# Optimization experiments

Measured on AMD Instinct MI355X. Metric: run time of the kernel, lower is better.

## Reference

```python
import jax, jax.numpy as jnp
import numpy as np
import math

H, C = 16, 4


def _clustering(x, alv, mu, log_var, log_prior, mi_estimation):
    # x: [B,h,L,D], alv: [B,h,L], mu/log_var: [h or 1, C, D], log_prior: [h or 1, C]
    B, Hh, L, D = x.shape
    z = x  # eval mode: no reparameterization noise
    zd = z[:, :, :, None, :]                       # [B,h,L,1,D]
    mu_b = mu[:, None, :, :]                       # [h,1,C,D]
    lv = log_var[:, None, :, :]
    var = jnp.exp(lv)
    lp = jax.nn.log_softmax(log_prior, axis=-1)    # [h,C]
    mse = (zd - mu_b) ** 2 / var                   # [B,h,L,C,D]
    log_pdf = -0.5 * mse.sum(-1) - 0.5 * lv.sum(-1) - D * math.pi  # [B,h,L,C]
    log_pdf = log_pdf + lp[:, None, :]
    shift = jax.lax.stop_gradient(log_pdf.max(axis=-1, keepdims=True))
    log_probs = jax.nn.log_softmax(log_pdf - shift + 5.0, axis=-1)
    cp = jnp.exp(log_probs)                        # cluster probs [B,h,L,C]
    lp_b = jnp.broadcast_to(lp[None, :, None, :], log_probs.shape)
    # F.kl_div(log_probs, prior) = prior * (log prior - log_probs)
    kl = (jnp.exp(lp_b) * (lp_b - log_probs)).sum(-1).mean(axis=(1, 2))
    alv5 = alv[:, :, :, None, None]
    avar = jnp.exp(alv5)
    kl = kl + 0.5 * (cp * (mse + avar / var + lv).sum(-1)).sum(-1).mean(axis=(1, 2))
    kl = kl - 0.5 * ((1.0 + alv5).sum(-1) * D).mean(axis=(1, 2, 3))
    eye = jnp.eye(L, dtype=x.dtype)
    div = jnp.einsum('bhqc,bhkc->bhqk', cp, cp)
    div = ((div - eye) ** 2) * (eye * 1.25 + (1.0 - eye) * 0.75)
    div_loss = div.mean(axis=(1, 2, 3))
    if mi_estimation:
        pdf = jnp.exp(log_pdf - jax.lax.stop_gradient(log_pdf.max())).sum(-1, keepdims=True)
        w = cp * pdf
        mi_probs = w / jnp.maximum(w.sum(axis=2, keepdims=True), 1e-6)  # L1 normalize over L
        mi_p = jnp.minimum(jnp.einsum('bilc,bjlc->blij', mi_probs, cp), 1.0)
        mask_h = 1.0 - jnp.eye(Hh, dtype=x.dtype)
        mi_loss = -(jnp.log(1.0 - mi_p + 1e-6) * mask_h).mean(axis=(1, 2, 3)) * 10.0
        aff = jnp.einsum('bhqc,bhkc->bhqk', cp, cp)
        diag = jnp.diagonal(jax.nn.log_softmax(aff, axis=-1), axis1=2, axis2=3)
        mi_loss = mi_loss - diag.mean(axis=(1, 2))
    else:
        mi_loss = jnp.zeros_like(kl)
    return z, cp, kl, div_loss, mi_loss


def _forward(query, key, value, Wq, bq, Wk, bk, Wv, bv, Wo, bo, Wsem, bsem,
             Whead, bhead, tok_mu, tok_log_var, tok_log_prior,
             head_mu, head_log_var, head_log_prior):
    B, L, D = query.shape
    Dk = D // H
    q = query @ Wq + bq
    k = key @ Wk + bk
    v = value @ Wv + bv
    alv = (q @ Wsem + bsem).transpose(0, 2, 1)                 # [B,H,L]
    qh = q.reshape(B, L, H, Dk).transpose(0, 2, 1, 3)          # [B,H,L,Dk]
    z, cp_q, kl_q, div_q, _ = _clustering(qh, alv, tok_mu, tok_log_var, tok_log_prior, False)
    kh = k.reshape(B, L, H, Dk).transpose(0, 2, 1, 3)
    vh = v.reshape(B, L, H, Dk).transpose(0, 2, 1, 3)
    cluster_mask = jnp.einsum('bhqc,bhkc->bhqk', cp_q, cp_q)   # token-cluster affinity mask
    scores = jnp.einsum('bhqd,bhkd->bhqk', z, kh) / math.sqrt(Dk)
    attn = jax.nn.softmax(scores, axis=-1) * cluster_mask
    attn = attn / (attn.sum(axis=-1, keepdims=True) + 1e-6)
    ctx = jnp.einsum('bhqk,bhkd->bhqd', attn, vh)              # [B,H,L,Dk]
    ctx_f = ctx.transpose(0, 2, 1, 3).reshape(B, L, D)
    alv_h = (ctx_f @ Whead + bhead).transpose(0, 2, 1)         # [B,H,L]
    _, cp_h, kl_h, div_h, mi = _clustering(ctx, alv_h, head_mu, head_log_var, head_log_prior, True)
    out = ctx_f @ Wo + bo
    return out, attn.mean(axis=1), kl_q + kl_h, div_q + div_h, mi


def setup_inputs() -> dict:
    key = jax.random.key(0)
    ks = jax.random.split(key, 12)
    B, L, D = 8, 512, 1024
    Dk = D // H
    s = 1.0 / math.sqrt(D)
    f32 = jnp.float32
    inp = {
        'query': jax.random.normal(ks[0], (B, L, D), f32),
        'key': jax.random.normal(ks[1], (B, L, D), f32),
        'value': jax.random.normal(ks[2], (B, L, D), f32),
        'Wq': jax.random.normal(ks[3], (D, D), f32) * s, 'bq': jnp.zeros((D,), f32),
        'Wk': jax.random.normal(ks[4], (D, D), f32) * s, 'bk': jnp.zeros((D,), f32),
        'Wv': jax.random.normal(ks[5], (D, D), f32) * s, 'bv': jnp.zeros((D,), f32),
        'Wo': jax.random.normal(ks[6], (D, D), f32) * s, 'bo': jnp.zeros((D,), f32),
        'Wsem': jax.random.normal(ks[7], (D, H), f32) * s, 'bsem': jnp.zeros((H,), f32),
        'Whead': jax.random.normal(ks[8], (D, H), f32) * s, 'bhead': jnp.zeros((H,), f32),
        'tok_mu': jax.random.normal(ks[9], (H, C, Dk), f32) * 0.1,
        'tok_log_var': jnp.zeros((H, C, Dk), f32),
        'tok_log_prior': jnp.full((H, C), math.log(1.0 / C), f32),
        'head_mu': jax.random.normal(ks[10], (1, C, Dk), f32) * 0.1,
        'head_log_var': jnp.zeros((1, C, Dk), f32),
        'head_log_prior': jnp.full((1, C), math.log(1.0 / C), f32),
    }
    return inp


def reference(query, key, value, Wq, bq, Wk, bk, Wv, bv, Wo, bo, Wsem, bsem,
              Whead, bhead, tok_mu, tok_log_var, tok_log_prior,
              head_mu, head_log_var, head_log_prior):
    return _forward(query, key, value, Wq, bq, Wk, bk, Wv, bv, Wo, bo, Wsem, bsem,
                    Whead, bhead, tok_mu, tok_log_var, tok_log_prior,
                    head_mu, head_log_var, head_log_prior)
```

## Files before the change

### kernel.cpp

```cpp
#include <hip/hip_runtime.h>
#include <math.h>

#define BB 8
#define LL 512
#define DD 1024
#define HH 16
#define CC 4
#define DK 64
#define NEG_DPI 201.06192982974676f

typedef __attribute__((ext_vector_type(8))) short short8;
typedef __attribute__((ext_vector_type(4))) float floatx4;
typedef __attribute__((ext_vector_type(8))) unsigned short u16x8;
typedef __attribute__((ext_vector_type(4))) unsigned short u16x4;

__device__ inline float block_sum256(float v, float* s_red) {
    int t = threadIdx.x;
    s_red[t] = v; __syncthreads();
    for (int off = 128; off > 0; off >>= 1) {
        if (t < off) s_red[t] += s_red[t + off];
        __syncthreads();
    }
    float r = s_red[0]; __syncthreads();
    return r;
}
__device__ inline float block_max256(float v, float* s_red) {
    int t = threadIdx.x;
    s_red[t] = v; __syncthreads();
    for (int off = 128; off > 0; off >>= 1) {
        if (t < off) s_red[t] = fmaxf(s_red[t], s_red[t + off]);
        __syncthreads();
    }
    float r = s_red[0]; __syncthreads();
    return r;
}
__device__ inline unsigned int fenc(float f) {
    unsigned int b = __float_as_uint(f);
    return (b & 0x80000000u) ? ~b : (b | 0x80000000u);
}
__device__ inline float fdec(unsigned int u) {
    return (u & 0x80000000u) ? __uint_as_float(u ^ 0x80000000u) : __uint_as_float(~u);
}
__device__ inline unsigned short f2bf(float x) {
    unsigned int u = __float_as_uint(x);
    return (unsigned short)((u + 0x7FFFu + ((u >> 16) & 1u)) >> 16);
}
__device__ inline float bf2f(unsigned short h) {
    return __uint_as_float((unsigned int)h << 16);
}

__global__ __launch_bounds__(256)
void convert_hilo(const float* __restrict__ x, unsigned short* __restrict__ hh,
                  unsigned short* __restrict__ ll) {
    int i = blockIdx.x * 256 + threadIdx.x;
    float4 v = ((const float4*)x)[i];
    u16x4 h, l;
    float c[4] = {v.x, v.y, v.z, v.w};
#pragma unroll
    for (int j = 0; j < 4; j++) {
        unsigned short hb = f2bf(c[j]);
        h[j] = hb;
        l[j] = f2bf(c[j] - bf2f(hb));
    }
    ((u16x4*)hh)[i] = h;
    ((u16x4*)ll)[i] = l;
}

__global__ __launch_bounds__(256)
void wconv4(const float* __restrict__ W0, const float* __restrict__ W1,
            const float* __restrict__ W2, const float* __restrict__ W3,
            unsigned short* __restrict__ Tbase) {
    __shared__ float tile[64][65];
    int z = blockIdx.z;
    const float* W = (z == 0) ? W0 : (z == 1) ? W1 : (z == 2) ? W2 : W3;
    const size_t WS = (size_t)DD * DD;
    unsigned short* Th = Tbase + (size_t)z * 2 * WS;
    unsigned short* Tl = Th + WS;
    int t = threadIdx.x;
    int n0 = blockIdx.x * 64, k0 = blockIdx.y * 64;
    int r = t >> 4, c4 = (t & 15) * 4;
#pragma unroll
    for (int rr = 0; rr < 64; rr += 16) {
        float4 v = *(const float4*)&W[(size_t)(k0 + r + rr) * DD + n0 + c4];
        tile[r + rr][c4 + 0] = v.x; tile[r + rr][c4 + 1] = v.y;
        tile[r + rr][c4 + 2] = v.z; tile[r + rr][c4 + 3] = v.w;
    }
    __syncthreads();
    int rn = t >> 2, kg = (t & 3) * 16;
    u16x8 oh[2], ol[2];
#pragma unroll
    for (int j = 0; j < 16; j++) {
        float x = tile[kg + j][rn];
        unsigned short hb = f2bf(x);
        oh[j >> 3][j & 7] = hb;
        ol[j >> 3][j & 7] = f2bf(x - bf2f(hb));
    }
    size_t o = (size_t)(n0 + rn) * DD + k0 + kg;
    *(u16x8*)&Th[o] = oh[0]; *(u16x8*)&Th[o + 8] = oh[1];
    *(u16x8*)&Tl[o] = ol[0]; *(u16x8*)&Tl[o + 8] = ol[1];
}

__device__ __forceinline__
void gemm_body(const unsigned short* __restrict__ Ah, const unsigned short* __restrict__ Al,
               const unsigned short* __restrict__ Bh, const unsigned short* __restrict__ Bl,
               const float* __restrict__ bias, float* __restrict__ C,
               unsigned short* __restrict__ Ch, unsigned short* __restrict__ Cl,
               int m0, int n0) {
    __shared__ unsigned short sAh[128 * 32];
    __shared__ unsigned short sAl[128 * 32];
    __shared__ unsigned short sBh[128 * 32];
    __shared__ unsigned short sBl[128 * 32];
    int t = threadIdx.x;
    int lane = t & 63, w = t >> 6;
    int wm = w >> 1, wn = w & 1;
    int lm = lane & 15, quad = lane >> 4;
    int srow = t >> 1, sk = (t & 1) * 16;

    const unsigned short* gAh = Ah + (size_t)(m0 + srow) * DD + sk;
    const unsigned short* gAl = Al + (size_t)(m0 + srow) * DD + sk;
    const unsigned short* gBh = Bh + (size_t)(n0 + srow) * DD + sk;
    const unsigned short* gBl = Bl + (size_t)(n0 + srow) * DD + sk;
    int f = (srow >> 1) & 3;
    int s0 = (t & 1) * 2;
    int ws0 = srow * 32 + ((s0 ^ f) * 8);
    int ws1 = srow * 32 + (((s0 | 1) ^ f) * 8);

    floatx4 acc[4][4] = {};
    u16x8 a0, a1, a2, a3, b0, b1, b2, b3;
    a0 = *(const u16x8*)(gAh);     a1 = *(const u16x8*)(gAh + 8);
    a2 = *(const u16x8*)(gAl);     a3 = *(const u16x8*)(gAl + 8);
    b0 = *(const u16x8*)(gBh);     b1 = *(const u16x8*)(gBh + 8);
    b2 = *(const u16x8*)(gBl);     b3 = *(const u16x8*)(gBl + 8);

    for (int kt = 0; kt < 32; kt++) {
        __syncthreads();
        *(u16x8*)&sAh[ws0] = a0; *(u16x8*)&sAh[ws1] = a1;
        *(u16x8*)&sAl[ws0] = a2; *(u16x8*)&sAl[ws1] = a3;
        *(u16x8*)&sBh[ws0] = b0; *(u16x8*)&sBh[ws1] = b1;
        *(u16x8*)&sBl[ws0] = b2; *(u16x8*)&sBl[ws1] = b3;
        __syncthreads();
        if (kt < 31) {
            int kb = (kt + 1) * 32;
            a0 = *(const u16x8*)(gAh + kb); a1 = *(const u16x8*)(gAh + kb + 8);
            a2 = *(const u16x8*)(gAl + kb); a3 = *(const u16x8*)(gAl + kb + 8);
            b0 = *(const u16x8*)(gBh + kb); b1 = *(const u16x8*)(gBh + kb + 8);
            b2 = *(const u16x8*)(gBl + kb); b3 = *(const u16x8*)(gBl + kb + 8);
        }

        short8 bhf[4], blf[4];
#pragma unroll
        for (int j = 0; j < 4; j++) {
            int nrow = wn * 64 + j * 16 + lm;
            int nb = nrow * 32 + ((quad ^ ((nrow >> 1) & 3)) * 8);
            bhf[j] = *(const short8*)&sBh[nb];
            blf[j] = *(const short8*)&sBl[nb];
        }
#pragma unroll
        for (int i = 0; i < 4; i++) {
            int arow = wm * 64 + i * 16 + lm;
            int ab = arow * 32 + ((quad ^ ((arow >> 1) & 3)) * 8);
            short8 ah = *(const short8*)&sAh[ab];
            short8 al = *(const short8*)&sAl[ab];
#pragma unroll
            for (int j = 0; j < 4; j++) {
                acc[i][j] = __builtin_amdgcn_mfma_f32_16x16x32_bf16(ah, bhf[j], acc[i][j], 0, 0, 0);
                acc[i][j] = __builtin_amdgcn_mfma_f32_16x16x32_bf16(ah, blf[j], acc[i][j], 0, 0, 0);
                acc[i][j] = __builtin_amdgcn_mfma_f32_16x16x32_bf16(al, bhf[j], acc[i][j], 0, 0, 0);
            }
        }
    }
#pragma unroll
    for (int i = 0; i < 4; i++) {
#pragma unroll
        for (int j = 0; j < 4; j++) {
            int n = n0 + wn * 64 + j * 16 + lm;
            float bv = bias[n];
#pragma unroll
            for (int r = 0; r < 4; r++) {
                int m = m0 + wm * 64 + i * 16 + quad * 4 + r;
                size_t idx = (size_t)m * DD + n;
                float val = acc[i][j][r] + bv;
                if (C) C[idx] = val;
                if (Ch) {
                    unsigned short hb = f2bf(val);
                    Ch[idx] = hb;
                    Cl[idx] = f2bf(val - bf2f(hb));
                }
            }
        }
    }
}

__global__ __launch_bounds__(256)
void mfma_gemm_bias(const unsigned short* __restrict__ Ah, const unsigned short* __restrict__ Al,
                    const unsigned short* __restrict__ Bh, const unsigned short* __restrict__ Bl,
                    const float* __restrict__ bias, float* __restrict__ C,
                    unsigned short* __restrict__ Ch, unsigned short* __restrict__ Cl) {
    int id = blockIdx.x;
    int xcd = id & 7, s = id >> 3;
    int y = xcd * 4 + (s >> 3);
    int x = s & 7;
    gemm_body(Ah, Al, Bh, Bl, bias, C, Ch, Cl, y * 128, x * 128);
}

__global__ __launch_bounds__(256)
void mfma_gemm_qkv(const unsigned short* __restrict__ ist3, const unsigned short* __restrict__ wbase,
                   const float* __restrict__ bq, const float* __restrict__ bk,
                   const float* __restrict__ bv, float* __restrict__ Cq,
                   unsigned short* __restrict__ obase) {
    int id = blockIdx.x;
    int xcd = id & 7, s = id >> 3;
    int p = xcd * 12 + (s >> 3);
    int x = s & 7;
    int z = p >> 5;
    int y = p & 31;
    const size_t NB = (size_t)BB * LL * DD;
    const size_t WS = (size_t)DD * DD;
    const unsigned short* Ah = ist3 + (size_t)z * 2 * NB;
    const unsigned short* Bh = wbase + (size_t)z * 2 * WS;
    const float* bias = (z == 0) ? bq : (z == 1) ? bk : bv;
    float* C = (z == 0) ? Cq : nullptr;
    unsigned short* Ch = obase + (size_t)z * 2 * NB;
    gemm_body(Ah, Ah + NB, Bh, Bh + WS, bias, C, Ch, Ch + NB, y * 128, x * 128);
}

__global__ __launch_bounds__(256)
void vt_prep2(const unsigned short* __restrict__ voh, const unsigned short* __restrict__ vol,
              unsigned short* __restrict__ vth, unsigned short* __restrict__ vtl) {
    __shared__ unsigned short tile[128 * 68];
    int t = threadIdx.x;
    int which = blockIdx.x & 1;
    int l0 = (blockIdx.x >> 1) * 128, h = blockIdx.y, b = blockIdx.z;
    const unsigned short* src = which ? vol : voh;
    unsigned short* dst = which ? vtl : vth;
#pragma unroll
    for (int i = 0; i < 8; i++) {
        int u = t + i * 256;
        int l = u >> 4, c4 = (u & 15) * 4;
        u16x4 v4 = *(const u16x4*)&src[((size_t)(b * LL + l0 + l)) * DD + h * DK + c4];
        tile[l * 68 + c4 + 0] = v4[0]; tile[l * 68 + c4 + 1] = v4[1];
        tile[l * 68 + c4 + 2] = v4[2]; tile[l * 68 + c4 + 3] = v4[3];
    }
    __syncthreads();
    size_t ob = ((size_t)(b * HH + h)) * DK * LL;
#pragma unroll
    for (int i = 0; i < 8; i++) {
        int u = t + i * 256;
        int d = u >> 5, lq = (u & 31) * 4;
        u16x4 o;
#pragma unroll
        for (int j = 0; j < 4; j++) o[j] = tile[(lq + j) * 68 + d];
        *(u16x4*)&dst[ob + (size_t)d * LL + l0 + lq] = o;
    }
}

__global__ __launch_bounds__(256)
void alv_gemm(const float* __restrict__ A, const float* __restrict__ Wp,
              const float* __restrict__ bias, float* __restrict__ alv) {
    __shared__ float As[16][65];
    __shared__ float Ws[64][17];
    int t = threadIdx.x;
    int m0 = blockIdx.x * 16;
    int r = t >> 4, hh = t & 15;
    float acc = 0.f;
    for (int kt = 0; kt < 16; kt++) {
        __syncthreads();
#pragma unroll
        for (int i = 0; i < 4; i++) {
            int e = t + i * 256;
            int rr = e >> 6, kk = e & 63;
            As[rr][kk] = A[(size_t)(m0 + rr) * DD + kt * 64 + kk];
        }
#pragma unroll
        for (int i = 0; i < 4; i++) {
            int e = t + i * 256;
            int kk = e >> 4, h2 = e & 15;
            Ws[kk][h2] = Wp[(size_t)(kt * 64 + kk) * HH + h2];
        }
        __syncthreads();
#pragma unroll
        for (int kk = 0; kk < 64; kk++) acc += As[r][kk] * Ws[kk][hh];
    }
    int m = m0 + r;
    int b = m >> 9, l = m & 511;
    alv[(size_t)(b * HH + hh) * LL + l] = acc + bias[hh];
}

__global__ __launch_bounds__(256)
void cluster_kernel(const float* __restrict__ zsrc, const float* __restrict__ alv,
                    const float* __restrict__ mu, const float* __restrict__ logvar,
                    const float* __restrict__ logprior,
                    float* __restrict__ cp_out, float* __restrict__ lpdf_out,
                    unsigned int* __restrict__ maxenc, float* __restrict__ kl_out,
                    int isHead) {
    __shared__ float s_mu[CC * DK], s_iv[CC * DK], s_lv[CC * DK];
    __shared__ float s_slv[CC], s_siv[CC], s_lp[CC];
    __shared__ float s_red[256];
    int t = threadIdx.x;
    int tile = blockIdx.x & 1;
    int bh = blockIdx.x >> 1;
    int h = bh & (HH - 1), b = bh >> 4;
    int hm = isHead ? 0 : h;

    {
        float m = mu[hm * CC * DK + t];
        float lv = logvar[hm * CC * DK + t];
        s_mu[t] = m; s_lv[t] = lv; s_iv[t] = expf(-lv);
    }
    __syncthreads();
    if (t < CC) {
        float slv = 0.f, siv = 0.f;
        for (int d = 0; d < DK; d++) { slv += s_lv[t * DK + d]; siv += s_iv[t * DK + d]; }
        s_slv[t] = slv; s_siv[t] = siv;
    }
    if (t == CC) {
        float x[CC];
        float m = -1e30f;
        for (int c = 0; c < CC; c++) { x[c] = logprior[hm * CC + c]; m = fmaxf(m, x[c]); }
        float se = 0.f;
        for (int c = 0; c < CC; c++) se += expf(x[c] - m);
        float lse = m + logf(se);
        for (int c = 0; c < CC; c++) s_lp[c] = x[c] - lse;
    }
    __syncthreads();

    int l = tile * 256 + t;
    const float* zp = zsrc + ((size_t)(b * LL + l)) * DD + h * DK;
    float acc[CC] = {0.f, 0.f, 0.f, 0.f};
    for (int d = 0; d < DK; d += 4) {
        float4 z4 = *(const float4*)(zp + d);
#pragma unroll
        for (int c = 0; c < CC; c++) {
            float d0 = z4.x - s_mu[c * DK + d];     acc[c] += d0 * d0 * s_iv[c * DK + d];
            float d1 = z4.y - s_mu[c * DK + d + 1]; acc[c] += d1 * d1 * s_iv[c * DK + d + 1];
            float d2 = z4.z - s_mu[c * DK + d + 2]; acc[c] += d2 * d2 * s_iv[c * DK + d + 2];
            float d3 = z4.w - s_mu[c * DK + d + 3]; acc[c] += d3 * d3 * s_iv[c * DK + d + 3];
        }
    }
    float lpdf[CC];
#pragma unroll
    for (int c = 0; c < CC; c++)
        lpdf[c] = -0.5f * acc[c] - 0.5f * s_slv[c] - NEG_DPI + s_lp[c];
    float m = fmaxf(fmaxf(lpdf[0], lpdf[1]), fmaxf(lpdf[2], lpdf[3]));
    float se = 0.f;
#pragma unroll
    for (int c = 0; c < CC; c++) se += expf(lpdf[c] - m);
    float lse = m + logf(se);
    float lprob[CC], cpv[CC];
    size_t idx = ((size_t)(bh * LL + l)) * CC;
#pragma unroll
    for (int c = 0; c < CC; c++) {
        lprob[c] = lpdf[c] - lse;
        cpv[c] = expf(lprob[c]);
        cp_out[idx + c] = cpv[c];
    }
    if (isHead) {
#pragma unroll
        for (int c = 0; c < CC; c++) lpdf_out[idx + c] = lpdf[c];
    }
    float alvv = alv[(size_t)bh * LL + l];
    float avar = expf(alvv);
    float t1 = 0.f, t2 = 0.f;
#pragma unroll
    for (int c = 0; c < CC; c++) {
        t1 += expf(s_lp[c]) * (s_lp[c] - lprob[c]);
        t2 += cpv[c] * (acc[c] + avar * s_siv[c] + s_slv[c]);
    }
    float klv = t1 + 0.5f * t2 - 0.5f * (float)DK * (1.0f + alvv);
    float tot = block_sum256(klv, s_red);
    if (t == 0) atomicAdd(kl_out + b, tot * (1.0f / (HH * LL)));
    if (isHead) {
        float mt = block_max256(m, s_red);
        if (t == 0) atomicMax(maxenc, fenc(mt));
    }
}

__global__ __launch_bounds__(256)
void pairstats_kernel(const float* __restrict__ cp, float* __restrict__ div_out,
                      float* __restrict__ mi_out, int isHead) {
    __shared__ float s_cp[LL * CC];
    __shared__ float s_red[256];
    int t = threadIdx.x;
    int bh = blockIdx.x >> 3;
    int seg = blockIdx.x & 7;
    int b = bh >> 4;
    const float* base = cp + (size_t)bh * LL * CC;
#pragma unroll
    for (int i = 0; i < 2; i++) {
        int e = t + i * 256;
        *(float4*)&s_cp[e * 4] = *(const float4*)&base[e * 4];
    }
    __syncthreads();

    int q = seg * 64 + (t >> 2);
    int ln = t & 3;
    float4 cq = *(float4*)&s_cp[q * 4];
    float divacc = 0.f, m = -1e30f, s = 0.f, selfdot = 0.f;
    for (int k = ln; k < LL; k += 4) {
        float4 ck = *(float4*)&s_cp[k * 4];
        float dot = cq.x * ck.x + cq.y * ck.y + cq.z * ck.z + cq.w * ck.w;
        float del = (k == q) ? 1.f : 0.f;
        float dd = dot - del;
        divacc += dd * dd * (0.75f + 0.5f * del);
        if (isHead) {
            if (dot > m) { s = s * expf(m - dot) + 1.f; m = dot; }
            else         { s += expf(dot - m); }
            if (k == q) selfdot = dot;
        }
    }
#pragma unroll
    for (int off = 1; off <= 2; off <<= 1) divacc += __shfl_xor(divacc, off, 64);
    float diag = 0.f;
    if (isHead) {
#pragma unroll
        for (int off = 1; off <= 2; off <<= 1) {
            float om = __shfl_xor(m, off, 64);
            float os = __shfl_xor(s, off, 64);
            float nm = fmaxf(m, om);
            s = s * expf(m - nm) + os * expf(om - nm);
            m = nm;
        }
#pragma unroll
        for (int off = 1; off <= 2; off <<= 1) selfdot += __shfl_xor(selfdot, off, 64);
        diag = selfdot - (m + logf(s));
    }
    float dtot = block_sum256(ln == 0 ? divacc : 0.f, s_red);
    if (t == 0) atomicAdd(div_out + b, dtot * (1.0f / ((float)HH * LL * LL)));
    if (isHead) {
        float gtot = block_sum256(ln == 0 ? diag : 0.f, s_red);
        if (t == 0) atomicAdd(mi_out + b, -gtot * (1.0f / (HH * LL)));
    }
}

__global__ __launch_bounds__(256)
void attn3_kernel(const unsigned short* __restrict__ qoh, const unsigned short* __restrict__ qol,
                  const unsigned short* __restrict__ koh, const unsigned short* __restrict__ kol,
                  const unsigned short* __restrict__ vth, const unsigned short* __restrict__ vtl,
                  const float* __restrict__ cpq,
                  float* __restrict__ ctxf, unsigned short* __restrict__ cxh,
                  unsigned short* __restrict__ cxl,
                  float* __restrict__ attn_h, int h0) {
    __shared__ __align__(16) char sbuf[33280];
    __shared__ float s_inv[16];
    float* S = (float*)sbuf;
    unsigned short* Ph = (unsigned short*)sbuf;
    unsigned short* Pl = Ph + 16 * 520;

    int t = threadIdx.x;
    int id = blockIdx.x;
    int xcd = id & 7;
    int sid = id >> 3;
    int qt = sid & 31;
    int combo = ((sid >> 5) << 3) | xcd;
    int hl = combo & 7;
    int b = combo >> 3;
    int h = h0 + hl;
    int q0 = qt * 16;
    int lane = t & 63, w = t >> 6;
    int lm = lane & 15, quad = lane >> 4;
    int bh = b * HH + h;

    size_t qbase = ((size_t)(b * LL + q0 + lm)) * DD + h * DK + quad * 8;
    short8 qah0 = *(const short8*)(qoh + qbase);
    short8 qah1 = *(const short8*)(qoh + qbase + 32);
    short8 qal0 = *(const short8*)(qol + qbase);
    short8 qal1 = *(const short8*)(qol + qbase + 32);

    floatx4 sa[8] = {};
#pragma unroll
    for (int j = 0; j < 8; j++) {
        int n0 = w * 128 + j * 16;
        size_t kbase = ((size_t)(b * LL + n0 + lm)) * DD + h * DK + quad * 8;
        short8 kbh0 = *(const short8*)(koh + kbase);
        short8 kbh1 = *(const short8*)(koh + kbase + 32);
        short8 kbl0 = *(const short8*)(kol + kbase);
        short8 kbl1 = *(const short8*)(kol + kbase + 32);
        sa[j] = __builtin_amdgcn_mfma_f32_16x16x32_bf16(qah0, kbh0, sa[j], 0, 0, 0);
        sa[j] = __builtin_amdgcn_mfma_f32_16x16x32_bf16(qah1, kbh1, sa[j], 0, 0, 0);
        sa[j] = __builtin_amdgcn_mfma_f32_16x16x32_bf16(qah0, kbl0, sa[j], 0, 0, 0);
        sa[j] = __builtin_amdgcn_mfma_f32_16x16x32_bf16(qah1, kbl1, sa[j], 0, 0, 0);
        sa[j] = __builtin_amdgcn_mfma_f32_16x16x32_bf16(qal0, kbh0, sa[j], 0, 0, 0);
        sa[j] = __builtin_amdgcn_mfma_f32_16x16x32_bf16(qal1, kbh1, sa[j], 0, 0, 0);
    }
#pragma unroll
    for (int j = 0; j < 8; j++) {
        int kc = w * 128 + j * 16 + lm;
#pragma unroll
        for (int r = 0; r < 4; r++)
            S[(quad * 4 + r) * 516 + kc] = sa[j][r] * 0.125f;
    }
    __syncthreads();

    {
        int r = t >> 4, ln = t & 15;
        const float4* cpb = (const float4*)(cpq + (size_t)bh * LL * CC);
        float m = -1e30f;
        for (int k = ln; k < LL; k += 16) m = fmaxf(m, S[r * 516 + k]);
#pragma unroll
        for (int off = 8; off > 0; off >>= 1) m = fmaxf(m, __shfl_xor(m, off, 16));
        float4 cq = cpb[q0 + r];
        float Z = 0.f, Sm = 0.f;
        for (int k = ln; k < LL; k += 16) {
            float e = expf(S[r * 516 + k] - m);
            float4 ck = cpb[k];
            float mask = cq.x * ck.x + cq.y * ck.y + cq.z * ck.z + cq.w * ck.w;
            float a = e * mask;
            Z += e; Sm += a;
            S[r * 516 + k] = a;
        }
#pragma unroll
        for (int off = 8; off > 0; off >>= 1) {
            Z += __shfl_xor(Z, off, 16);
            Sm += __shfl_xor(Sm, off, 16);
        }
        if (ln == 0) s_inv[r] = 1.f / (Sm + 1e-6f * Z);
    }
    __syncthreads();

    float4 pv[8];
#pragma unroll
    for (int i = 0; i < 8; i++) {
        int e = t + i * 256;
        int r2 = e >> 7, k4 = (e & 127) * 4;
        float4 p = *(float4*)&S[r2 * 516 + k4];
        float inv = s_inv[r2];
        p.x *= inv; p.y *= inv; p.z *= inv; p.w *= inv;
        pv[i] = p;
        *(float4*)&attn_h[(((size_t)((b * 8 + hl) * LL + q0 + r2)) * LL) + k4] = p;
    }
    __syncthreads();
#pragma unroll
    for (int i = 0; i < 8; i++) {
        int e = t + i * 256;
        int r2 = e >> 7, k4 = (e & 127) * 4;
        float c[4] = {pv[i].x, pv[i].y, pv[i].z, pv[i].w};
        u16x4 hv, lv;
#pragma unroll
        for (int j = 0; j < 4; j++) {
            unsigned short hb = f2bf(c[j]);
            hv[j] = hb;
            lv[j] = f2bf(c[j] - bf2f(hb));
        }
        *(u16x4*)&Ph[r2 * 520 + k4] = hv;
        *(u16x4*)&Pl[r2 * 520 + k4] = lv;
    }
    __syncthreads();

    int dn = w * 16 + lm;
    const unsigned short* vrh = vth + ((size_t)bh * DK + dn) * LL;
    const unsigned short* vrl = vtl + ((size_t)bh * DK + dn) * LL;
    floatx4 ca = {};
#pragma unroll
    for (int kc = 0; kc < 16; kc++) {
        int kb = kc * 32 + quad * 8;
        short8 pah = *(const short8*)&Ph[lm * 520 + kb];
        short8 pal = *(const short8*)&Pl[lm * 520 + kb];
        short8 vbh = *(const short8*)(vrh + kb);
        short8 vbl = *(const short8*)(vrl + kb);
        ca = __builtin_amdgcn_mfma_f32_16x16x32_bf16(pah, vbh, ca, 0, 0, 0);
        ca = __builtin_amdgcn_mfma_f32_16x16x32_bf16(pah, vbl, ca, 0, 0, 0);
        ca = __builtin_amdgcn_mfma_f32_16x16x32_bf16(pal, vbh, ca, 0, 0, 0);
    }
#pragma unroll
    for (int r = 0; r < 4; r++) {
        float val = ca[r];
        size_t idx = ((size_t)(b * LL + q0 + quad * 4 + r)) * DD + h * DK + dn;
        ctxf[idx] = val;
        unsigned short hb = f2bf(val);
        cxh[idx] = hb;
        cxl[idx] = f2bf(val - bf2f(hb));
    }
}

__global__ __launch_bounds__(256)
void attn_reduce(const float* __restrict__ attn_h, float* __restrict__ attn_out,
                 int accumulate) {
    int e = blockIdx.x * 256 + threadIdx.x;
    int b = e >> 16;
    int rem = e & 65535;
    float4 s = {0.f, 0.f, 0.f, 0.f};
#pragma unroll
    for (int hl = 0; hl < 8; hl++) {
        float4 v = ((const float4*)attn_h)[(((size_t)(b * 8 + hl)) << 16) + rem];
        s.x += v.x; s.y += v.y; s.z += v.z; s.w += v.w;
    }
    float4* o = (float4*)attn_out + (((size_t)b) << 16) + rem;
    const float sc = 1.0f / (float)HH;
    float4 prev = {0.f, 0.f, 0.f, 0.f};
    if (accumulate) prev = *o;
    prev.x += s.x * sc; prev.y += s.y * sc; prev.z += s.z * sc; prev.w += s.w * sc;
    *o = prev;
}

__global__ __launch_bounds__(256)
void wsum_kernel(const float* __restrict__ lpdf, const float* __restrict__ cp,
                 const unsigned int* __restrict__ maxenc,
                 float* __restrict__ pdf_out, float* __restrict__ wsum_out) {
    __shared__ float s_red[256];
    int t = threadIdx.x;
    int bh = blockIdx.x;
    float M = fdec(*maxenc);
    float a[CC] = {0.f, 0.f, 0.f, 0.f};
    for (int li = 0; li < 2; li++) {
        int l = t + li * 256;
        size_t idx = ((size_t)bh * LL + l) * CC;
        float p0 = expf(lpdf[idx + 0] - M);
        float p1 = expf(lpdf[idx + 1] - M);
        float p2 = expf(lpdf[idx + 2] - M);
        float p3 = expf(lpdf[idx + 3] - M);
        float pd = p0 + p1 + p2 + p3;
        pdf_out[(size_t)bh * LL + l] = pd;
        a[0] += cp[idx + 0] * pd; a[1] += cp[idx + 1] * pd;
        a[2] += cp[idx + 2] * pd; a[3] += cp[idx + 3] * pd;
    }
#pragma unroll
    for (int c = 0; c < CC; c++) {
        float tot = block_sum256(a[c], s_red);
        if (t == 0) wsum_out[bh * CC + c] = tot;
    }
}

__global__ __launch_bounds__(256)
void mi_kernel(const float* __restrict__ cp, const float* __restrict__ pdf,
               const float* __restrict__ wsum, float* __restrict__ mi_out) {
    __shared__ float s_q[HH * CC];
    __shared__ float s_c[HH * CC];
    __shared__ float s_red[256];
    int t = threadIdx.x;
    int b = blockIdx.x >> 9;
    int l = blockIdx.x & 511;
    if (t < HH * CC) {
        int i = t >> 2, c = t & 3;
        float cpv = cp[((size_t)(b * HH + i) * LL + l) * CC + c];
        s_c[t] = cpv;
        float w = cpv * pdf[(size_t)(b * HH + i) * LL + l];
        float ws = wsum[(b * HH + i) * CC + c];
        s_q[t] = w / fmaxf(ws, 1e-6f);
    }
    __syncthreads();
    int i = t >> 4, j = t & 15;
    float sdot = 0.f;
#pragma unroll
    for (int c = 0; c < CC; c++) sdot += s_q[i * 4 + c] * s_c[j * 4 + c];
    float mi_p = fminf(sdot, 1.f);
    float val = (i != j) ? logf(1.f - mi_p + 1e-6f) : 0.f;
    float tot = block_sum256(val, s_red);
    if (t == 0) atomicAdd(mi_out + b, -10.f * tot * (1.0f / ((float)LL * HH * HH)));
}

extern "C" void kernel_launch(void* const* d_in, const int* in_sizes, int n_in,
                              void* d_out, int out_size, void* d_ws, size_t ws_size,
                              hipStream_t stream) {
    (void)in_sizes; (void)n_in; (void)out_size; (void)ws_size;
    const float* query  = (const float*)d_in[0];
    const float* key    = (const float*)d_in[1];
    const float* value  = (const float*)d_in[2];
    const float* Wq     = (const float*)d_in[3];
    const float* bq     = (const float*)d_in[4];
    const float* Wk     = (const float*)d_in[5];
    const float* bk     = (const float*)d_in[6];
    const float* Wv     = (const float*)d_in[7];
    const float* bv     = (const float*)d_in[8];
    const float* Wo     = (const float*)d_in[9];
    const float* bo     = (const float*)d_in[10];
    const float* Wsem   = (const float*)d_in[11];
    const float* bsem   = (const float*)d_in[12];
    const float* Whead  = (const float*)d_in[13];
    const float* bhead  = (const float*)d_in[14];
    const float* tokmu  = (const float*)d_in[15];
    const float* toklv  = (const float*)d_in[16];
    const float* toklp  = (const float*)d_in[17];
    const float* headmu = (const float*)d_in[18];
    const float* headlv = (const float*)d_in[19];
    const float* headlp = (const float*)d_in[20];

    float* ws   = (float*)d_ws;
    const size_t NBLD = (size_t)BB * LL * DD;
    float* q    = ws;
    float* ctxf = ws + NBLD;
    float* alvq = ws + 2 * NBLD;
    float* alvh = alvq + (size_t)BB * HH * LL;
    float* cpq  = alvh + (size_t)BB * HH * LL;
    float* cph  = cpq + (size_t)BB * HH * LL * CC;
    float* lpdfh= cph + (size_t)BB * HH * LL * CC;
    float* pdfb = lpdfh + (size_t)BB * HH * LL * CC;
    float* wsumb= pdfb + (size_t)BB * HH * LL;
    unsigned int* maxenc = (unsigned int*)(wsumb + (size_t)BB * HH * CC);
    float* scr3 = (float*)(maxenc + 4);

    unsigned short* us = (unsigned short*)(scr3 + (size_t)BB * 8 * LL * LL);
    const size_t WSZ = (size_t)DD * DD;
    unsigned short* ist_h = us;
    unsigned short* ist_l = ist_h + NBLD;
    unsigned short* qoh = ist_l + NBLD;
    unsigned short* qol = qoh + NBLD;
    unsigned short* koh = qol + NBLD;
    unsigned short* kol = koh + NBLD;
    unsigned short* voh = kol + NBLD;
    unsigned short* vol = voh + NBLD;
    unsigned short* vth = vol + NBLD;
    unsigned short* vtl = vth + NBLD;
    unsigned short* wqh = vtl + NBLD;
    unsigned short* wql = wqh + WSZ;
    unsigned short* wkh = wql + WSZ;
    unsigned short* wkl = wkh + WSZ;
    unsigned short* wvh = wkl + WSZ;
    unsigned short* wvl = wvh + WSZ;
    unsigned short* woh = wvl + WSZ;
    unsigned short* wol = woh + WSZ;

    unsigned short* ist3 = (unsigned short*)scr3;
    float* attn_h = scr3;

    float* out      = (float*)d_out;
    float* attn_out = out + NBLD;
    float* kl_out   = attn_out + (size_t)BB * LL * LL;
    float* div_out  = kl_out + BB;
    float* mi_out   = div_out + BB;

    hipMemsetAsync(kl_out, 0, 3 * BB * sizeof(float), stream);
    hipMemsetAsync(maxenc, 0, sizeof(unsigned int), stream);

    wconv4<<<dim3(16, 16, 4), 256, 0, stream>>>(Wq, Wk, Wv, Wo, wqh);

    convert_hilo<<<NBLD / 1024, 256, 0, stream>>>(query, ist3,            ist3 + NBLD);
    convert_hilo<<<NBLD / 1024, 256, 0, stream>>>(key,   ist3 + 2 * NBLD, ist3 + 3 * NBLD);
    convert_hilo<<<NBLD / 1024, 256, 0, stream>>>(value, ist3 + 4 * NBLD, ist3 + 5 * NBLD);
    mfma_gemm_qkv<<<dim3(768), 256, 0, stream>>>(
        ist3, wqh, bq, bk, bv, q, qoh);

    vt_prep2<<<dim3(2 * LL / 128, HH, BB), 256, 0, stream>>>(voh, vol, vth, vtl);

    alv_gemm<<<BB * LL / 16, 256, 0, stream>>>(q, Wsem, bsem, alvq);
    cluster_kernel<<<BB * HH * 2, 256, 0, stream>>>(q, alvq, tokmu, toklv, toklp,
                                                    cpq, nullptr, nullptr, kl_out, 0);
    pairstats_kernel<<<BB * HH * 8, 256, 0, stream>>>(cpq, div_out, nullptr, 0);

    for (int h0 = 0; h0 < HH; h0 += 8) {
        attn3_kernel<<<dim3(2048), 256, 0, stream>>>(
            qoh, qol, koh, kol, vth, vtl, cpq, ctxf, ist_h, ist_l, attn_h, h0);
        attn_reduce<<<BB * LL * LL / 4 / 256, 256, 0, stream>>>(
            attn_h, attn_out, h0 > 0 ? 1 : 0);
    }

    alv_gemm<<<BB * LL / 16, 256, 0, stream>>>(ctxf, Whead, bhead, alvh);
    cluster_kernel<<<BB * HH * 2, 256, 0, stream>>>(ctxf, alvh, headmu, headlv, headlp,
                                                    cph, lpdfh, maxenc, kl_out, 1);
    pairstats_kernel<<<BB * HH * 8, 256, 0, stream>>>(cph, div_out, mi_out, 1);
    wsum_kernel<<<BB * HH, 256, 0, stream>>>(lpdfh, cph, maxenc, pdfb, wsumb);
    mi_kernel<<<BB * LL, 256, 0, stream>>>(cph, pdfb, wsumb, mi_out);
    mfma_gemm_bias<<<dim3(256), 256, 0, stream>>>(
        ist_h, ist_l, woh, wol, bo, out, nullptr, nullptr);
}
```

Before: 764.0 us.

## Fuse fp32-to-bf16 hi/lo split into GEMM A-operand loads

Removes the three convert_hilo launches for query/key/value and the hi/lo writes of the attention context. The QKV and output GEMMs now read fp32 A directly and split it into bf16 hi/lo in registers while prefetching. This saves writing and re-reading the bf16 copies of the activations (roughly 6 NBLD shorts plus 2 for ctx). In exchange each GEMM block redoes the split for A tiles shared across N-blocks, and its global loads are twice as wide in bytes.

```diff
diff --git a/kernel.cpp b/kernel.cpp
--- a/kernel.cpp
+++ b/kernel.cpp
@@ -48,22 +48,14 @@
 __device__ inline float bf2f(unsigned short h) {
     return __uint_as_float((unsigned int)h << 16);
 }
-
-__global__ __launch_bounds__(256)
-void convert_hilo(const float* __restrict__ x, unsigned short* __restrict__ hh,
-                  unsigned short* __restrict__ ll) {
-    int i = blockIdx.x * 256 + threadIdx.x;
-    float4 v = ((const float4*)x)[i];
-    u16x4 h, l;
-    float c[4] = {v.x, v.y, v.z, v.w};
-#pragma unroll
-    for (int j = 0; j < 4; j++) {
+__device__ inline void split8(const float4 x, const float4 y, u16x8& h, u16x8& l) {
+    float c[8] = {x.x, x.y, x.z, x.w, y.x, y.y, y.z, y.w};
+#pragma unroll
+    for (int j = 0; j < 8; j++) {
         unsigned short hb = f2bf(c[j]);
         h[j] = hb;
         l[j] = f2bf(c[j] - bf2f(hb));
     }
-    ((u16x4*)hh)[i] = h;
-    ((u16x4*)ll)[i] = l;
 }
 
 __global__ __launch_bounds__(256)
@@ -100,8 +92,10 @@
     *(u16x8*)&Tl[o] = ol[0]; *(u16x8*)&Tl[o + 8] = ol[1];
 }
 
+template<int AFP32>
 __device__ __forceinline__
-void gemm_body(const unsigned short* __restrict__ Ah, const unsigned short* __restrict__ Al,
+void gemm_body(const float* __restrict__ Af,
+               const unsigned short* __restrict__ Ah, const unsigned short* __restrict__ Al,
                const unsigned short* __restrict__ Bh, const unsigned short* __restrict__ Bl,
                const float* __restrict__ bias, float* __restrict__ C,
                unsigned short* __restrict__ Ch, unsigned short* __restrict__ Cl,
@@ -116,8 +110,9 @@
     int lm = lane & 15, quad = lane >> 4;
     int srow = t >> 1, sk = (t & 1) * 16;
 
-    const unsigned short* gAh = Ah + (size_t)(m0 + srow) * DD + sk;
-    const unsigned short* gAl = Al + (size_t)(m0 + srow) * DD + sk;
+    const float* gAf = AFP32 ? (Af + (size_t)(m0 + srow) * DD + sk) : nullptr;
+    const unsigned short* gAh = AFP32 ? nullptr : (Ah + (size_t)(m0 + srow) * DD + sk);
+    const unsigned short* gAl = AFP32 ? nullptr : (Al + (size_t)(m0 + srow) * DD + sk);
     const unsigned short* gBh = Bh + (size_t)(n0 + srow) * DD + sk;
     const unsigned short* gBl = Bl + (size_t)(n0 + srow) * DD + sk;
     int f = (srow >> 1) & 3;
@@ -127,8 +122,17 @@
 
     floatx4 acc[4][4] = {};
     u16x8 a0, a1, a2, a3, b0, b1, b2, b3;
-    a0 = *(const u16x8*)(gAh);     a1 = *(const u16x8*)(gAh + 8);
-    a2 = *(const u16x8*)(gAl);     a3 = *(const u16x8*)(gAl + 8);
+    if (AFP32) {
+        float4 f0 = *(const float4*)(gAf);
+        float4 f1 = *(const float4*)(gAf + 4);
+        float4 f2 = *(const float4*)(gAf + 8);
+        float4 f3 = *(const float4*)(gAf + 12);
+        split8(f0, f1, a0, a2);
+        split8(f2, f3, a1, a3);
+    } else {
+        a0 = *(const u16x8*)(gAh);     a1 = *(const u16x8*)(gAh + 8);
+        a2 = *(const u16x8*)(gAl);     a3 = *(const u16x8*)(gAl + 8);
+    }
     b0 = *(const u16x8*)(gBh);     b1 = *(const u16x8*)(gBh + 8);
     b2 = *(const u16x8*)(gBl);     b3 = *(const u16x8*)(gBl + 8);
 
@@ -141,8 +145,17 @@
         __syncthreads();
         if (kt < 31) {
             int kb = (kt + 1) * 32;
-            a0 = *(const u16x8*)(gAh + kb); a1 = *(const u16x8*)(gAh + kb + 8);
-            a2 = *(const u16x8*)(gAl + kb); a3 = *(const u16x8*)(gAl + kb + 8);
+            if (AFP32) {
+                float4 f0 = *(const float4*)(gAf + kb);
+                float4 f1 = *(const float4*)(gAf + kb + 4);
+                float4 f2 = *(const float4*)(gAf + kb + 8);
+                float4 f3 = *(const float4*)(gAf + kb + 12);
+                split8(f0, f1, a0, a2);
+                split8(f2, f3, a1, a3);
+            } else {
+                a0 = *(const u16x8*)(gAh + kb); a1 = *(const u16x8*)(gAh + kb + 8);
+                a2 = *(const u16x8*)(gAl + kb); a3 = *(const u16x8*)(gAl + kb + 8);
+            }
             b0 = *(const u16x8*)(gBh + kb); b1 = *(const u16x8*)(gBh + kb + 8);
             b2 = *(const u16x8*)(gBl + kb); b3 = *(const u16x8*)(gBl + kb + 8);
         }
@@ -192,19 +205,19 @@
 }
 
 __global__ __launch_bounds__(256)
-void mfma_gemm_bias(const unsigned short* __restrict__ Ah, const unsigned short* __restrict__ Al,
+void mfma_gemm_bias(const float* __restrict__ Af,
                     const unsigned short* __restrict__ Bh, const unsigned short* __restrict__ Bl,
-                    const float* __restrict__ bias, float* __restrict__ C,
-                    unsigned short* __restrict__ Ch, unsigned short* __restrict__ Cl) {
+                    const float* __restrict__ bias, float* __restrict__ C) {
     int id = blockIdx.x;
     int xcd = id & 7, s = id >> 3;
     int y = xcd * 4 + (s >> 3);
     int x = s & 7;
-    gemm_body(Ah, Al, Bh, Bl, bias, C, Ch, Cl, y * 128, x * 128);
-}
-
-__global__ __launch_bounds__(256)
-void mfma_gemm_qkv(const unsigned short* __restrict__ ist3, const unsigned short* __restrict__ wbase,
+    gemm_body<1>(Af, nullptr, nullptr, Bh, Bl, bias, C, nullptr, nullptr, y * 128, x * 128);
+}
+
+__global__ __launch_bounds__(256)
+void mfma_gemm_qkv(const float* __restrict__ qin, const float* __restrict__ kin,
+                   const float* __restrict__ vin, const unsigned short* __restrict__ wbase,
                    const float* __restrict__ bq, const float* __restrict__ bk,
                    const float* __restrict__ bv, float* __restrict__ Cq,
                    unsigned short* __restrict__ obase) {
@@ -216,12 +229,12 @@
     int y = p & 31;
     const size_t NB = (size_t)BB * LL * DD;
     const size_t WS = (size_t)DD * DD;
-    const unsigned short* Ah = ist3 + (size_t)z * 2 * NB;
+    const float* Af = (z == 0) ? qin : (z == 1) ? kin : vin;
     const unsigned short* Bh = wbase + (size_t)z * 2 * WS;
     const float* bias = (z == 0) ? bq : (z == 1) ? bk : bv;
     float* C = (z == 0) ? Cq : nullptr;
     unsigned short* Ch = obase + (size_t)z * 2 * NB;
-    gemm_body(Ah, Ah + NB, Bh, Bh + WS, bias, C, Ch, Ch + NB, y * 128, x * 128);
+    gemm_body<1>(Af, nullptr, nullptr, Bh, Bh + WS, bias, C, Ch, Ch + NB, y * 128, x * 128);
 }
 
 __global__ __launch_bounds__(256)
@@ -437,8 +450,7 @@
                   const unsigned short* __restrict__ koh, const unsigned short* __restrict__ kol,
                   const unsigned short* __restrict__ vth, const unsigned short* __restrict__ vtl,
                   const float* __restrict__ cpq,
-                  float* __restrict__ ctxf, unsigned short* __restrict__ cxh,
-                  unsigned short* __restrict__ cxl,
+                  float* __restrict__ ctxf,
                   float* __restrict__ attn_h, int h0) {
     __shared__ __align__(16) char sbuf[33280];
     __shared__ float s_inv[16];
@@ -562,14 +574,8 @@
         ca = __builtin_amdgcn_mfma_f32_16x16x32_bf16(pal, vbh, ca, 0, 0, 0);
     }
 #pragma unroll
-    for (int r = 0; r < 4; r++) {
-        float val = ca[r];
-        size_t idx = ((size_t)(b * LL + q0 + quad * 4 + r)) * DD + h * DK + dn;
-        ctxf[idx] = val;
-        unsigned short hb = f2bf(val);
-        cxh[idx] = hb;
-        cxl[idx] = f2bf(val - bf2f(hb));
-    }
+    for (int r = 0; r < 4; r++)
+        ctxf[((size_t)(b * LL + q0 + quad * 4 + r)) * DD + h * DK + dn] = ca[r];
 }
 
 __global__ __launch_bounds__(256)
@@ -686,13 +692,11 @@
     float* pdfb = lpdfh + (size_t)BB * HH * LL * CC;
     float* wsumb= pdfb + (size_t)BB * HH * LL;
     unsigned int* maxenc = (unsigned int*)(wsumb + (size_t)BB * HH * CC);
-    float* scr3 = (float*)(maxenc + 4);
-
-    unsigned short* us = (unsigned short*)(scr3 + (size_t)BB * 8 * LL * LL);
+    float* attn_h = (float*)(maxenc + 4);
+
+    unsigned short* us = (unsigned short*)(attn_h + (size_t)BB * 8 * LL * LL);
     const size_t WSZ = (size_t)DD * DD;
-    unsigned short* ist_h = us;
-    unsigned short* ist_l = ist_h + NBLD;
-    unsigned short* qoh = ist_l + NBLD;
+    unsigned short* qoh = us;
     unsigned short* qol = qoh + NBLD;
     unsigned short* koh = qol + NBLD;
     unsigned short* kol = koh + NBLD;
@@ -701,16 +705,8 @@
     unsigned short* vth = vol + NBLD;
     unsigned short* vtl = vth + NBLD;
     unsigned short* wqh = vtl + NBLD;
-    unsigned short* wql = wqh + WSZ;
-    unsigned short* wkh = wql + WSZ;
-    unsigned short* wkl = wkh + WSZ;
-    unsigned short* wvh = wkl + WSZ;
-    unsigned short* wvl = wvh + WSZ;
-    unsigned short* woh = wvl + WSZ;
+    unsigned short* woh = wqh + 6 * WSZ;
     unsigned short* wol = woh + WSZ;
-
-    unsigned short* ist3 = (unsigned short*)scr3;
-    float* attn_h = scr3;
 
     float* out      = (float*)d_out;
     float* attn_out = out + NBLD;
@@ -723,11 +719,8 @@
 
     wconv4<<<dim3(16, 16, 4), 256, 0, stream>>>(Wq, Wk, Wv, Wo, wqh);
 
-    convert_hilo<<<NBLD / 1024, 256, 0, stream>>>(query, ist3,            ist3 + NBLD);
-    convert_hilo<<<NBLD / 1024, 256, 0, stream>>>(key,   ist3 + 2 * NBLD, ist3 + 3 * NBLD);
-    convert_hilo<<<NBLD / 1024, 256, 0, stream>>>(value, ist3 + 4 * NBLD, ist3 + 5 * NBLD);
     mfma_gemm_qkv<<<dim3(768), 256, 0, stream>>>(
-        ist3, wqh, bq, bk, bv, q, qoh);
+        query, key, value, wqh, bq, bk, bv, q, qoh);
 
     vt_prep2<<<dim3(2 * LL / 128, HH, BB), 256, 0, stream>>>(voh, vol, vth, vtl);
 
@@ -738,7 +731,7 @@
 
     for (int h0 = 0; h0 < HH; h0 += 8) {
         attn3_kernel<<<dim3(2048), 256, 0, stream>>>(
-            qoh, qol, koh, kol, vth, vtl, cpq, ctxf, ist_h, ist_l, attn_h, h0);
+            qoh, qol, koh, kol, vth, vtl, cpq, ctxf, attn_h, h0);
         attn_reduce<<<BB * LL * LL / 4 / 256, 256, 0, stream>>>(
             attn_h, attn_out, h0 > 0 ? 1 : 0);
     }
@@ -750,5 +743,5 @@
     wsum_kernel<<<BB * HH, 256, 0, stream>>>(lpdfh, cph, maxenc, pdfb, wsumb);
     mi_kernel<<<BB * LL, 256, 0, stream>>>(cph, pdfb, wsumb, mi_out);
     mfma_gemm_bias<<<dim3(256), 256, 0, stream>>>(
-        ist_h, ist_l, woh, wol, bo, out, nullptr, nullptr);
-}
+        ctxf, woh, wol, bo, out);
+}
```

Result: faster. 749.0 us (-2.0%).
